# Performance work log

Hardware: AMD Instinct MI355X
Metric: run time of the kernel (lower is better)

Reference implementation:

```python
import jax, jax.numpy as jnp
import numpy as np

BN_EPS = 1e-5
LEAKY_SLOPE = 0.01

N_TOTAL, FEAT_DIM = 100000, 128
N_BATCH, K = 50000, 16
EMBED_DIM = 128


def setup_inputs() -> dict:
    key = jax.random.key(0)
    k1, k2, k3 = jax.random.split(key, 3)
    raw_features = jax.random.normal(k1, (N_TOTAL, FEAT_DIM), dtype=jnp.float32)
    weight = jax.random.normal(k2, (FEAT_DIM, EMBED_DIM), dtype=jnp.float32) * (1.0 / np.sqrt(FEAT_DIM))
    gamma = jnp.ones((EMBED_DIM,), dtype=jnp.float32)
    beta = jnp.zeros((EMBED_DIM,), dtype=jnp.float32)
    neigh_idx = jax.random.randint(k3, (N_BATCH, K), 0, N_TOTAL, dtype=jnp.int64)
    return {"raw_features": raw_features, "weight": weight, "gamma": gamma,
            "beta": beta, "neigh_idx": neigh_idx}


def reference(raw_features, weight, gamma, beta, neigh_idx):
    # Mean aggregation over sampled neighbors: [N_BATCH, K, F] -> [N_BATCH, F]
    neigh_feats = jnp.mean(raw_features[neigh_idx], axis=1)
    # Dense transform: [N_BATCH, EMBED_DIM]
    x = neigh_feats @ weight
    # BatchNorm1d (training mode: batch statistics, biased variance)
    mean = jnp.mean(x, axis=0)
    var = jnp.var(x, axis=0)
    x = (x - mean) * jax.lax.rsqrt(var + BN_EPS) * gamma + beta
    # LeakyReLU (default negative_slope=0.01)
    return jnp.where(x >= 0, x, LEAKY_SLOPE * x)
```

## Files before the change

### kernel.cpp

```cpp
#include <hip/hip_runtime.h>
#include <hip/hip_bf16.h>


#define NTOTAL 100000
#define FEAT   128
#define NB     50000
#define KNEI   16
#define NTILES (NB / 16)

#define OFF_STATS 0
#define OFF_WT    1024
#define OFF_RAWB  33792
#define OFF_XB    (33792 + 25600000)
#define WS_NEEDED (OFF_XB + 12800000)

typedef float f32x4 __attribute__((ext_vector_type(4)));
typedef short bf16x8 __attribute__((ext_vector_type(8)));

__device__ __forceinline__ unsigned short f2bf(float f) {
    union { float f; unsigned u; } v; v.f = f;
    unsigned r = v.u + 0x7FFF + ((v.u >> 16) & 1);
    return (unsigned short)(r >> 16);
}

#define WT_LD 136
#define A_LD  136

__global__ __launch_bounds__(256) void enc_conv(
    const float* __restrict__ raw, const float* __restrict__ W,
    unsigned short* __restrict__ rawb, unsigned short* __restrict__ Wt,
    float* __restrict__ gstats)
{
    const int t = threadIdx.x;
    if (blockIdx.x < 64) {
        int e = blockIdx.x * 256 + t;
        int n = e >> 7, k = e & 127;
        Wt[e] = f2bf(W[k * FEAT + n]);
    }
    if (blockIdx.x == 64 && t < 2 * FEAT) gstats[t] = 0.f;

    const float4* raw4 = (const float4*)raw;
    ushort4* rb4 = (ushort4*)rawb;
    const int NQ = NTOTAL * FEAT / 4;
    for (int e = blockIdx.x * 256 + t; e < NQ; e += gridDim.x * 256) {
        float4 v = raw4[e];
        ushort4 b;
        b.x = f2bf(v.x); b.y = f2bf(v.y); b.z = f2bf(v.z); b.w = f2bf(v.w);
        rb4[e] = b;
    }
}

__global__ __launch_bounds__(256, 4) void enc_gemm_b(
    const unsigned short* __restrict__ rawb, const unsigned short* __restrict__ Wt,
    const int* __restrict__ idx, unsigned short* __restrict__ xb,
    float* __restrict__ gstats)
{
    __shared__ unsigned short sWt[128 * WT_LD];
    __shared__ unsigned short sA[16 * A_LD];
    __shared__ int sidx[256];

    const int t = threadIdx.x;

    #pragma unroll
    for (int i = 0; i < 8; ++i) {
        int e = t + i * 256;
        int n = e >> 4, c = e & 15;
        *(uint4*)&sWt[n * WT_LD + c * 8] = *(const uint4*)&Wt[n * 128 + c * 8];
    }

    const int lane = t & 63;
    const int wv = t >> 6;
    const int ln = lane & 15;
    const int qd = lane >> 4;
    const int c2 = t & 15;
    const int g  = t >> 4;
    const int n0 = wv * 32 + ln, n1 = n0 + 16;

    float s1a = 0.f, s2a = 0.f, s1b = 0.f, s2b = 0.f;

    for (int tile = blockIdx.x; tile < NTILES; tile += gridDim.x) {
        const int i0 = tile * 16;
        __syncthreads();
        sidx[t] = idx[i0 * KNEI + t];
        __syncthreads();

        {
            const int* ip = &sidx[g * KNEI];
            uint4 v[16];
            #pragma unroll
            for (int k = 0; k < KNEI; ++k)
                v[k] = *(const uint4*)&rawb[(size_t)ip[k] * FEAT + c2 * 8];
            float a0=0.f,a1=0.f,a2=0.f,a3=0.f,a4=0.f,a5=0.f,a6=0.f,a7=0.f;
            #pragma unroll
            for (int k = 0; k < KNEI; ++k) {
                a0 += __uint_as_float(v[k].x << 16);
                a1 += __uint_as_float(v[k].x & 0xFFFF0000u);
                a2 += __uint_as_float(v[k].y << 16);
                a3 += __uint_as_float(v[k].y & 0xFFFF0000u);
                a4 += __uint_as_float(v[k].z << 16);
                a5 += __uint_as_float(v[k].z & 0xFFFF0000u);
                a6 += __uint_as_float(v[k].w << 16);
                a7 += __uint_as_float(v[k].w & 0xFFFF0000u);
            }
            uint4 b;
            b.x = (unsigned)f2bf(a0 * 0.0625f) | ((unsigned)f2bf(a1 * 0.0625f) << 16);
            b.y = (unsigned)f2bf(a2 * 0.0625f) | ((unsigned)f2bf(a3 * 0.0625f) << 16);
            b.z = (unsigned)f2bf(a4 * 0.0625f) | ((unsigned)f2bf(a5 * 0.0625f) << 16);
            b.w = (unsigned)f2bf(a6 * 0.0625f) | ((unsigned)f2bf(a7 * 0.0625f) << 16);
            *(uint4*)&sA[g * A_LD + c2 * 8] = b;
        }
        __syncthreads();

        f32x4 acc0 = {0.f, 0.f, 0.f, 0.f}, acc1 = {0.f, 0.f, 0.f, 0.f};
        #pragma unroll
        for (int kt = 0; kt < 4; ++kt) {
            const int k0 = kt * 32 + qd * 8;
            bf16x8 a  = *(const bf16x8*)&sA[ln * A_LD + k0];
            bf16x8 b0 = *(const bf16x8*)&sWt[n0 * WT_LD + k0];
            bf16x8 b1 = *(const bf16x8*)&sWt[n1 * WT_LD + k0];
            acc0 = __builtin_amdgcn_mfma_f32_16x16x32_bf16(a, b0, acc0, 0, 0, 0);
            acc1 = __builtin_amdgcn_mfma_f32_16x16x32_bf16(a, b1, acc1, 0, 0, 0);
        }

        #pragma unroll
        for (int ri = 0; ri < 4; ++ri) {
            const int row = i0 + qd * 4 + ri;
            float v0 = acc0[ri], v1 = acc1[ri];
            xb[row * FEAT + n0] = f2bf(v0);
            xb[row * FEAT + n1] = f2bf(v1);
            s1a += v0; s2a += v0 * v0;
            s1b += v1; s2b += v1 * v1;
        }
    }

    s1a += __shfl_down(s1a, 32); s1a += __shfl_down(s1a, 16);
    s2a += __shfl_down(s2a, 32); s2a += __shfl_down(s2a, 16);
    s1b += __shfl_down(s1b, 32); s1b += __shfl_down(s1b, 16);
    s2b += __shfl_down(s2b, 32); s2b += __shfl_down(s2b, 16);
    if (qd == 0) {
        atomicAdd(&gstats[n0], s1a);
        atomicAdd(&gstats[FEAT + n0], s2a);
        atomicAdd(&gstats[n1], s1b);
        atomicAdd(&gstats[FEAT + n1], s2b);
    }
}

__global__ __launch_bounds__(256) void enc_bn_b(
    const unsigned short* __restrict__ xb, float* __restrict__ out,
    const float* __restrict__ gstats,
    const float* __restrict__ gamma, const float* __restrict__ beta)
{
    __shared__ float sScale[FEAT], sShift[FEAT];
    const int t = threadIdx.x;
    if (t < FEAT) {
        float s1 = gstats[t], s2 = gstats[FEAT + t];
        float mean = s1 * (1.0f / NB);
        float var = s2 * (1.0f / NB) - mean * mean;
        float sc = gamma[t] * rsqrtf(var + 1e-5f);
        sScale[t] = sc;
        sShift[t] = beta[t] - mean * sc;
    }
    __syncthreads();

    const int f8 = (t & 15) * 8;
    const float4 sc0 = *(const float4*)&sScale[f8], sc1 = *(const float4*)&sScale[f8 + 4];
    const float4 sh0 = *(const float4*)&sShift[f8], sh1 = *(const float4*)&sShift[f8 + 4];

    const uint4* x4 = (const uint4*)xb;
    float4* o4 = (float4*)out;
    const int total8 = NB * FEAT / 8;
    for (int e = blockIdx.x * 256 + t; e < total8; e += gridDim.x * 256) {
        uint4 v = x4[e];
        float4 r0, r1; float y;
        y = __uint_as_float(v.x << 16)        * sc0.x + sh0.x; r0.x = (y >= 0.f) ? y : 0.01f * y;
        y = __uint_as_float(v.x & 0xFFFF0000u)* sc0.y + sh0.y; r0.y = (y >= 0.f) ? y : 0.01f * y;
        y = __uint_as_float(v.y << 16)        * sc0.z + sh0.z; r0.z = (y >= 0.f) ? y : 0.01f * y;
        y = __uint_as_float(v.y & 0xFFFF0000u)* sc0.w + sh0.w; r0.w = (y >= 0.f) ? y : 0.01f * y;
        y = __uint_as_float(v.z << 16)        * sc1.x + sh1.x; r1.x = (y >= 0.f) ? y : 0.01f * y;
        y = __uint_as_float(v.z & 0xFFFF0000u)* sc1.y + sh1.y; r1.y = (y >= 0.f) ? y : 0.01f * y;
        y = __uint_as_float(v.w << 16)        * sc1.z + sh1.z; r1.z = (y >= 0.f) ? y : 0.01f * y;
        y = __uint_as_float(v.w & 0xFFFF0000u)* sc1.w + sh1.w; r1.w = (y >= 0.f) ? y : 0.01f * y;
        o4[e * 2] = r0; o4[e * 2 + 1] = r1;
    }
}

__global__ __launch_bounds__(256, 4) void enc_gemm_f(
    const float* __restrict__ raw, const float* __restrict__ W,
    const int* __restrict__ idx, float* __restrict__ out,
    float* __restrict__ gstats)
{
    __shared__ unsigned short sWt[128 * WT_LD];
    __shared__ unsigned short sA[16 * A_LD];
    __shared__ int sidx[256];
    const int t = threadIdx.x;
    #pragma unroll 4
    for (int i = 0; i < 64; ++i) {
        int e = t + i * 256;
        int f = e >> 7, n = e & 127;
        sWt[n * WT_LD + f] = f2bf(W[e]);
    }
    const int lane = t & 63, wv = t >> 6, ln = lane & 15, qd = lane >> 4;
    const int c = t & 31, g = t >> 5;
    const int n0 = wv * 32 + ln, n1 = n0 + 16;
    float s1a = 0.f, s2a = 0.f, s1b = 0.f, s2b = 0.f;
    const float4* raw4 = (const float4*)raw;
    for (int tile = blockIdx.x; tile < NTILES; tile += gridDim.x) {
        const int i0 = tile * 16;
        __syncthreads();
        sidx[t] = idx[i0 * KNEI + t];
        __syncthreads();
        #pragma unroll
        for (int rr = 0; rr < 2; ++rr) {
            const int r = g * 2 + rr;
            const int* ip = &sidx[r * KNEI];
            float4 acc = {0.f, 0.f, 0.f, 0.f};
            #pragma unroll
            for (int k = 0; k < KNEI; ++k) {
                float4 v = raw4[(size_t)ip[k] * 32 + c];
                acc.x += v.x; acc.y += v.y; acc.z += v.z; acc.w += v.w;
            }
            ushort4 b;
            b.x = f2bf(acc.x * 0.0625f); b.y = f2bf(acc.y * 0.0625f);
            b.z = f2bf(acc.z * 0.0625f); b.w = f2bf(acc.w * 0.0625f);
            *(ushort4*)&sA[r * A_LD + c * 4] = b;
        }
        __syncthreads();
        f32x4 acc0 = {0.f, 0.f, 0.f, 0.f}, acc1 = {0.f, 0.f, 0.f, 0.f};
        #pragma unroll
        for (int kt = 0; kt < 4; ++kt) {
            const int k0 = kt * 32 + qd * 8;
            bf16x8 a  = *(const bf16x8*)&sA[ln * A_LD + k0];
            bf16x8 b0 = *(const bf16x8*)&sWt[n0 * WT_LD + k0];
            bf16x8 b1 = *(const bf16x8*)&sWt[n1 * WT_LD + k0];
            acc0 = __builtin_amdgcn_mfma_f32_16x16x32_bf16(a, b0, acc0, 0, 0, 0);
            acc1 = __builtin_amdgcn_mfma_f32_16x16x32_bf16(a, b1, acc1, 0, 0, 0);
        }
        #pragma unroll
        for (int ri = 0; ri < 4; ++ri) {
            const int row = i0 + qd * 4 + ri;
            float v0 = acc0[ri], v1 = acc1[ri];
            out[row * FEAT + n0] = v0;
            out[row * FEAT + n1] = v1;
            s1a += v0; s2a += v0 * v0;
            s1b += v1; s2b += v1 * v1;
        }
    }
    s1a += __shfl_down(s1a, 32); s1a += __shfl_down(s1a, 16);
    s2a += __shfl_down(s2a, 32); s2a += __shfl_down(s2a, 16);
    s1b += __shfl_down(s1b, 32); s1b += __shfl_down(s1b, 16);
    s2b += __shfl_down(s2b, 32); s2b += __shfl_down(s2b, 16);
    if (qd == 0) {
        atomicAdd(&gstats[n0], s1a);
        atomicAdd(&gstats[FEAT + n0], s2a);
        atomicAdd(&gstats[n1], s1b);
        atomicAdd(&gstats[FEAT + n1], s2b);
    }
}

__global__ __launch_bounds__(256) void enc_bn_f(
    float* __restrict__ out, const float* __restrict__ gstats,
    const float* __restrict__ gamma, const float* __restrict__ beta)
{
    __shared__ float sScale[FEAT], sShift[FEAT];
    const int t = threadIdx.x;
    if (t < FEAT) {
        float s1 = gstats[t], s2 = gstats[FEAT + t];
        float mean = s1 * (1.0f / NB);
        float var = s2 * (1.0f / NB) - mean * mean;
        float sc = gamma[t] * rsqrtf(var + 1e-5f);
        sScale[t] = sc;
        sShift[t] = beta[t] - mean * sc;
    }
    __syncthreads();
    const int f4 = (t & 31) * 4;
    const float4 sc = *(const float4*)&sScale[f4];
    const float4 sh = *(const float4*)&sShift[f4];
    const int total4 = NB * FEAT / 4;
    float4* o4 = (float4*)out;
    for (int e = blockIdx.x * 256 + t; e < total4; e += gridDim.x * 256) {
        float4 v = o4[e];
        float4 r; float y;
        y = v.x * sc.x + sh.x; r.x = (y >= 0.f) ? y : 0.01f * y;
        y = v.y * sc.y + sh.y; r.y = (y >= 0.f) ? y : 0.01f * y;
        y = v.z * sc.z + sh.z; r.z = (y >= 0.f) ? y : 0.01f * y;
        y = v.w * sc.w + sh.w; r.w = (y >= 0.f) ? y : 0.01f * y;
        o4[e] = r;
    }
}

extern "C" void kernel_launch(void* const* d_in, const int* in_sizes, int n_in,
                              void* d_out, int out_size, void* d_ws, size_t ws_size,
                              hipStream_t stream) {
    const float* raw   = (const float*)d_in[0];
    const float* W     = (const float*)d_in[1];
    const float* gamma = (const float*)d_in[2];
    const float* beta  = (const float*)d_in[3];
    const int*   idx   = (const int*)d_in[4];
    float* out = (float*)d_out;

    char* ws = (char*)d_ws;
    float* gstats = (float*)(ws + OFF_STATS);

    if (ws_size >= WS_NEEDED) {
        unsigned short* Wt   = (unsigned short*)(ws + OFF_WT);
        unsigned short* rawb = (unsigned short*)(ws + OFF_RAWB);
        unsigned short* xb   = (unsigned short*)(ws + OFF_XB);
        enc_conv<<<2048, 256, 0, stream>>>(raw, W, rawb, Wt, gstats);
        enc_gemm_b<<<1024, 256, 0, stream>>>(rawb, Wt, idx, xb, gstats);
        enc_bn_b<<<1024, 256, 0, stream>>>(xb, out, gstats, gamma, beta);
    } else {
        hipMemsetAsync(gstats, 0, 2 * FEAT * sizeof(float), stream);
        enc_gemm_f<<<1024, 256, 0, stream>>>(raw, W, idx, out, gstats);
        enc_bn_f<<<1024, 256, 0, stream>>>(out, gstats, gamma, beta);
    }
}
```

Baseline: 151.9 us.

## Split gather and GEMM into separate kernels using fp16 packed accumulation

Replaces the fused bf16 gather+GEMM kernel with a standalone gather kernel that sums neighbor rows with packed half2 adds (tree reduction) and writes fp16 neighbor means to workspace. A separate MFMA f16 GEMM kernel then holds the weights in registers, writes fp32 output directly, and accumulates BN statistics, and BN is applied in place. The goal is to cut ALU conversion work in the gather, avoid LDS syncs, and drop the bf16 intermediate of x. The cost is an extra kernel launch and an extra round trip of the neighbor-feature buffer. fp16 accumulation risks precision loss and overflow, and the in-place BN adds a read-modify-write of the fp32 output.

```diff
diff --git a/kernel.cpp b/kernel.cpp
--- a/kernel.cpp
+++ b/kernel.cpp
@@ -1,5 +1,6 @@
 #include <hip/hip_runtime.h>
 #include <hip/hip_bf16.h>
+#include <hip/hip_fp16.h>
 
 
 #define NTOTAL 100000
@@ -10,12 +11,13 @@
 
 #define OFF_STATS 0
 #define OFF_WT    1024
-#define OFF_RAWB  33792
-#define OFF_XB    (33792 + 25600000)
-#define WS_NEEDED (OFF_XB + 12800000)
+#define OFF_RAWH  33792
+#define OFF_NF    (33792 + 25600000)
+#define WS_NEEDED (OFF_NF + 12800000)
 
 typedef float f32x4 __attribute__((ext_vector_type(4)));
 typedef short bf16x8 __attribute__((ext_vector_type(8)));
+typedef _Float16 f16x8 __attribute__((ext_vector_type(8)));
 
 __device__ __forceinline__ unsigned short f2bf(float f) {
     union { float f; unsigned u; } v; v.f = f;
@@ -23,111 +25,117 @@
     return (unsigned short)(r >> 16);
 }
 
-#define WT_LD 136
-#define A_LD  136
+__device__ __forceinline__ unsigned h2add(unsigned a, unsigned b) {
+    union { unsigned u; __half2 h; } x, y, r;
+    x.u = a; y.u = b; r.h = __hadd2(x.h, y.h);
+    return r.u;
+}
+__device__ __forceinline__ unsigned h2scale16(unsigned a) {
+    union { unsigned u; __half2 h; } x, c, r;
+    x.u = a; c.u = 0x2C002C00u;
+    r.h = __hmul2(x.h, c.h);
+    return r.u;
+}
 
 __global__ __launch_bounds__(256) void enc_conv(
     const float* __restrict__ raw, const float* __restrict__ W,
-    unsigned short* __restrict__ rawb, unsigned short* __restrict__ Wt,
+    unsigned short* __restrict__ rawh, unsigned short* __restrict__ Wt,
     float* __restrict__ gstats)
 {
     const int t = threadIdx.x;
     if (blockIdx.x < 64) {
         int e = blockIdx.x * 256 + t;
         int n = e >> 7, k = e & 127;
-        Wt[e] = f2bf(W[k * FEAT + n]);
+        union { unsigned short s; __half h; } c; c.h = __float2half(W[k * FEAT + n]);
+        Wt[e] = c.s;
     }
     if (blockIdx.x == 64 && t < 2 * FEAT) gstats[t] = 0.f;
 
     const float4* raw4 = (const float4*)raw;
-    ushort4* rb4 = (ushort4*)rawb;
+    uint2* rh = (uint2*)rawh;
     const int NQ = NTOTAL * FEAT / 4;
     for (int e = blockIdx.x * 256 + t; e < NQ; e += gridDim.x * 256) {
         float4 v = raw4[e];
-        ushort4 b;
-        b.x = f2bf(v.x); b.y = f2bf(v.y); b.z = f2bf(v.z); b.w = f2bf(v.w);
-        rb4[e] = b;
-    }
-}
-
-__global__ __launch_bounds__(256, 4) void enc_gemm_b(
-    const unsigned short* __restrict__ rawb, const unsigned short* __restrict__ Wt,
-    const int* __restrict__ idx, unsigned short* __restrict__ xb,
-    float* __restrict__ gstats)
-{
-    __shared__ unsigned short sWt[128 * WT_LD];
-    __shared__ unsigned short sA[16 * A_LD];
-    __shared__ int sidx[256];
-
-    const int t = threadIdx.x;
-
+        union { unsigned u; __half2 h; } lo, hi;
+        lo.h = __float22half2_rn(make_float2(v.x, v.y));
+        hi.h = __float22half2_rn(make_float2(v.z, v.w));
+        uint2 o; o.x = lo.u; o.y = hi.u;
+        rh[e] = o;
+    }
+}
+
+__global__ __launch_bounds__(256, 5) void enc_gather(
+    const unsigned short* __restrict__ rawh, const int* __restrict__ idx,
+    unsigned short* __restrict__ nf)
+{
+    const int t = threadIdx.x;
+    const int lane = t & 63;
+    const int w = (blockIdx.x * 256 + t) >> 6;
+    const int r0 = w * 4;
+    const int s = lane >> 4, c = lane & 15;
+
+    const int iv = idx[r0 * KNEI + lane];
+
+    uint4 v[16];
     #pragma unroll
-    for (int i = 0; i < 8; ++i) {
-        int e = t + i * 256;
-        int n = e >> 4, c = e & 15;
-        *(uint4*)&sWt[n * WT_LD + c * 8] = *(const uint4*)&Wt[n * 128 + c * 8];
-    }
-
+    for (int k = 0; k < KNEI; ++k) {
+        int ik = __shfl(iv, s * 16 + k);
+        v[k] = *(const uint4*)&rawh[(size_t)ik * FEAT + c * 8];
+    }
+    #pragma unroll
+    for (int st = 8; st >= 1; st >>= 1) {
+        #pragma unroll
+        for (int k = 0; k < 8; ++k) {
+            if (k < st) {
+                v[k].x = h2add(v[k].x, v[k + st].x);
+                v[k].y = h2add(v[k].y, v[k + st].y);
+                v[k].z = h2add(v[k].z, v[k + st].z);
+                v[k].w = h2add(v[k].w, v[k + st].w);
+            }
+        }
+    }
+    uint4 o;
+    o.x = h2scale16(v[0].x); o.y = h2scale16(v[0].y);
+    o.z = h2scale16(v[0].z); o.w = h2scale16(v[0].w);
+    *(uint4*)&nf[(size_t)(r0 + s) * FEAT + c * 8] = o;
+}
+
+__global__ __launch_bounds__(256, 4) void enc_mm(
+    const unsigned short* __restrict__ nf, const unsigned short* __restrict__ Wt,
+    float* __restrict__ out, float* __restrict__ gstats)
+{
+    const int t = threadIdx.x;
     const int lane = t & 63;
     const int wv = t >> 6;
-    const int ln = lane & 15;
-    const int qd = lane >> 4;
-    const int c2 = t & 15;
-    const int g  = t >> 4;
+    const int ln = lane & 15, qd = lane >> 4;
     const int n0 = wv * 32 + ln, n1 = n0 + 16;
+
+    f16x8 b0[4], b1[4];
+    #pragma unroll
+    for (int kt = 0; kt < 4; ++kt) {
+        const int k0 = kt * 32 + qd * 8;
+        b0[kt] = *(const f16x8*)&Wt[n0 * FEAT + k0];
+        b1[kt] = *(const f16x8*)&Wt[n1 * FEAT + k0];
+    }
 
     float s1a = 0.f, s2a = 0.f, s1b = 0.f, s2b = 0.f;
 
     for (int tile = blockIdx.x; tile < NTILES; tile += gridDim.x) {
         const int i0 = tile * 16;
-        __syncthreads();
-        sidx[t] = idx[i0 * KNEI + t];
-        __syncthreads();
-
-        {
-            const int* ip = &sidx[g * KNEI];
-            uint4 v[16];
-            #pragma unroll
-            for (int k = 0; k < KNEI; ++k)
-                v[k] = *(const uint4*)&rawb[(size_t)ip[k] * FEAT + c2 * 8];
-            float a0=0.f,a1=0.f,a2=0.f,a3=0.f,a4=0.f,a5=0.f,a6=0.f,a7=0.f;
-            #pragma unroll
-            for (int k = 0; k < KNEI; ++k) {
-                a0 += __uint_as_float(v[k].x << 16);
-                a1 += __uint_as_float(v[k].x & 0xFFFF0000u);
-                a2 += __uint_as_float(v[k].y << 16);
-                a3 += __uint_as_float(v[k].y & 0xFFFF0000u);
-                a4 += __uint_as_float(v[k].z << 16);
-                a5 += __uint_as_float(v[k].z & 0xFFFF0000u);
-                a6 += __uint_as_float(v[k].w << 16);
-                a7 += __uint_as_float(v[k].w & 0xFFFF0000u);
-            }
-            uint4 b;
-            b.x = (unsigned)f2bf(a0 * 0.0625f) | ((unsigned)f2bf(a1 * 0.0625f) << 16);
-            b.y = (unsigned)f2bf(a2 * 0.0625f) | ((unsigned)f2bf(a3 * 0.0625f) << 16);
-            b.z = (unsigned)f2bf(a4 * 0.0625f) | ((unsigned)f2bf(a5 * 0.0625f) << 16);
-            b.w = (unsigned)f2bf(a6 * 0.0625f) | ((unsigned)f2bf(a7 * 0.0625f) << 16);
-            *(uint4*)&sA[g * A_LD + c2 * 8] = b;
-        }
-        __syncthreads();
-
         f32x4 acc0 = {0.f, 0.f, 0.f, 0.f}, acc1 = {0.f, 0.f, 0.f, 0.f};
         #pragma unroll
         for (int kt = 0; kt < 4; ++kt) {
             const int k0 = kt * 32 + qd * 8;
-            bf16x8 a  = *(const bf16x8*)&sA[ln * A_LD + k0];
-            bf16x8 b0 = *(const bf16x8*)&sWt[n0 * WT_LD + k0];
-            bf16x8 b1 = *(const bf16x8*)&sWt[n1 * WT_LD + k0];
-            acc0 = __builtin_amdgcn_mfma_f32_16x16x32_bf16(a, b0, acc0, 0, 0, 0);
-            acc1 = __builtin_amdgcn_mfma_f32_16x16x32_bf16(a, b1, acc1, 0, 0, 0);
-        }
-
+            f16x8 a = *(const f16x8*)&nf[(size_t)(i0 + ln) * FEAT + k0];
+            acc0 = __builtin_amdgcn_mfma_f32_16x16x32_f16(a, b0[kt], acc0, 0, 0, 0);
+            acc1 = __builtin_amdgcn_mfma_f32_16x16x32_f16(a, b1[kt], acc1, 0, 0, 0);
+        }
         #pragma unroll
         for (int ri = 0; ri < 4; ++ri) {
             const int row = i0 + qd * 4 + ri;
             float v0 = acc0[ri], v1 = acc1[ri];
-            xb[row * FEAT + n0] = f2bf(v0);
-            xb[row * FEAT + n1] = f2bf(v1);
+            out[row * FEAT + n0] = v0;
+            out[row * FEAT + n1] = v1;
             s1a += v0; s2a += v0 * v0;
             s1b += v1; s2b += v1 * v1;
         }
@@ -145,119 +153,7 @@
     }
 }
 
-__global__ __launch_bounds__(256) void enc_bn_b(
-    const unsigned short* __restrict__ xb, float* __restrict__ out,
-    const float* __restrict__ gstats,
-    const float* __restrict__ gamma, const float* __restrict__ beta)
-{
-    __shared__ float sScale[FEAT], sShift[FEAT];
-    const int t = threadIdx.x;
-    if (t < FEAT) {
-        float s1 = gstats[t], s2 = gstats[FEAT + t];
-        float mean = s1 * (1.0f / NB);
-        float var = s2 * (1.0f / NB) - mean * mean;
-        float sc = gamma[t] * rsqrtf(var + 1e-5f);
-        sScale[t] = sc;
-        sShift[t] = beta[t] - mean * sc;
-    }
-    __syncthreads();
-
-    const int f8 = (t & 15) * 8;
-    const float4 sc0 = *(const float4*)&sScale[f8], sc1 = *(const float4*)&sScale[f8 + 4];
-    const float4 sh0 = *(const float4*)&sShift[f8], sh1 = *(const float4*)&sShift[f8 + 4];
-
-    const uint4* x4 = (const uint4*)xb;
-    float4* o4 = (float4*)out;
-    const int total8 = NB * FEAT / 8;
-    for (int e = blockIdx.x * 256 + t; e < total8; e += gridDim.x * 256) {
-        uint4 v = x4[e];
-        float4 r0, r1; float y;
-        y = __uint_as_float(v.x << 16)        * sc0.x + sh0.x; r0.x = (y >= 0.f) ? y : 0.01f * y;
-        y = __uint_as_float(v.x & 0xFFFF0000u)* sc0.y + sh0.y; r0.y = (y >= 0.f) ? y : 0.01f * y;
-        y = __uint_as_float(v.y << 16)        * sc0.z + sh0.z; r0.z = (y >= 0.f) ? y : 0.01f * y;
-        y = __uint_as_float(v.y & 0xFFFF0000u)* sc0.w + sh0.w; r0.w = (y >= 0.f) ? y : 0.01f * y;
-        y = __uint_as_float(v.z << 16)        * sc1.x + sh1.x; r1.x = (y >= 0.f) ? y : 0.01f * y;
-        y = __uint_as_float(v.z & 0xFFFF0000u)* sc1.y + sh1.y; r1.y = (y >= 0.f) ? y : 0.01f * y;
-        y = __uint_as_float(v.w << 16)        * sc1.z + sh1.z; r1.z = (y >= 0.f) ? y : 0.01f * y;
-        y = __uint_as_float(v.w & 0xFFFF0000u)* sc1.w + sh1.w; r1.w = (y >= 0.f) ? y : 0.01f * y;
-        o4[e * 2] = r0; o4[e * 2 + 1] = r1;
-    }
-}
-
-__global__ __launch_bounds__(256, 4) void enc_gemm_f(
-    const float* __restrict__ raw, const float* __restrict__ W,
-    const int* __restrict__ idx, float* __restrict__ out,
-    float* __restrict__ gstats)
-{
-    __shared__ unsigned short sWt[128 * WT_LD];
-    __shared__ unsigned short sA[16 * A_LD];
-    __shared__ int sidx[256];
-    const int t = threadIdx.x;
-    #pragma unroll 4
-    for (int i = 0; i < 64; ++i) {
-        int e = t + i * 256;
-        int f = e >> 7, n = e & 127;
-        sWt[n * WT_LD + f] = f2bf(W[e]);
-    }
-    const int lane = t & 63, wv = t >> 6, ln = lane & 15, qd = lane >> 4;
-    const int c = t & 31, g = t >> 5;
-    const int n0 = wv * 32 + ln, n1 = n0 + 16;
-    float s1a = 0.f, s2a = 0.f, s1b = 0.f, s2b = 0.f;
-    const float4* raw4 = (const float4*)raw;
-    for (int tile = blockIdx.x; tile < NTILES; tile += gridDim.x) {
-        const int i0 = tile * 16;
-        __syncthreads();
-        sidx[t] = idx[i0 * KNEI + t];
-        __syncthreads();
-        #pragma unroll
-        for (int rr = 0; rr < 2; ++rr) {
-            const int r = g * 2 + rr;
-            const int* ip = &sidx[r * KNEI];
-            float4 acc = {0.f, 0.f, 0.f, 0.f};
-            #pragma unroll
-            for (int k = 0; k < KNEI; ++k) {
-                float4 v = raw4[(size_t)ip[k] * 32 + c];
-                acc.x += v.x; acc.y += v.y; acc.z += v.z; acc.w += v.w;
-            }
-            ushort4 b;
-            b.x = f2bf(acc.x * 0.0625f); b.y = f2bf(acc.y * 0.0625f);
-            b.z = f2bf(acc.z * 0.0625f); b.w = f2bf(acc.w * 0.0625f);
-            *(ushort4*)&sA[r * A_LD + c * 4] = b;
-        }
-        __syncthreads();
-        f32x4 acc0 = {0.f, 0.f, 0.f, 0.f}, acc1 = {0.f, 0.f, 0.f, 0.f};
-        #pragma unroll
-        for (int kt = 0; kt < 4; ++kt) {
-            const int k0 = kt * 32 + qd * 8;
-            bf16x8 a  = *(const bf16x8*)&sA[ln * A_LD + k0];
-            bf16x8 b0 = *(const bf16x8*)&sWt[n0 * WT_LD + k0];
-            bf16x8 b1 = *(const bf16x8*)&sWt[n1 * WT_LD + k0];
-            acc0 = __builtin_amdgcn_mfma_f32_16x16x32_bf16(a, b0, acc0, 0, 0, 0);
-            acc1 = __builtin_amdgcn_mfma_f32_16x16x32_bf16(a, b1, acc1, 0, 0, 0);
-        }
-        #pragma unroll
-        for (int ri = 0; ri < 4; ++ri) {
-            const int row = i0 + qd * 4 + ri;
-            float v0 = acc0[ri], v1 = acc1[ri];
-            out[row * FEAT + n0] = v0;
-            out[row * FEAT + n1] = v1;
-            s1a += v0; s2a += v0 * v0;
-            s1b += v1; s2b += v1 * v1;
-        }
-    }
-    s1a += __shfl_down(s1a, 32); s1a += __shfl_down(s1a, 16);
-    s2a += __shfl_down(s2a, 32); s2a += __shfl_down(s2a, 16);
-    s1b += __shfl_down(s1b, 32); s1b += __shfl_down(s1b, 16);
-    s2b += __shfl_down(s2b, 32); s2b += __shfl_down(s2b, 16);
-    if (qd == 0) {
-        atomicAdd(&gstats[n0], s1a);
-        atomicAdd(&gstats[FEAT + n0], s2a);
-        atomicAdd(&gstats[n1], s1b);
-        atomicAdd(&gstats[FEAT + n1], s2b);
-    }
-}
-
-__global__ __launch_bounds__(256) void enc_bn_f(
+__global__ __launch_bounds__(256) void enc_bn(
     float* __restrict__ out, const float* __restrict__ gstats,
     const float* __restrict__ gamma, const float* __restrict__ beta)
 {
@@ -288,6 +184,81 @@
     }
 }
 
+#define WT_LD 136
+#define A_LD  136
+__global__ __launch_bounds__(256, 4) void enc_gemm_f(
+    const float* __restrict__ raw, const float* __restrict__ W,
+    const int* __restrict__ idx, float* __restrict__ out,
+    float* __restrict__ gstats)
+{
+    __shared__ unsigned short sWt[128 * WT_LD];
+    __shared__ unsigned short sA[16 * A_LD];
+    __shared__ int sidx[256];
+    const int t = threadIdx.x;
+    #pragma unroll 4
+    for (int i = 0; i < 64; ++i) {
+        int e = t + i * 256;
+        int f = e >> 7, n = e & 127;
+        sWt[n * WT_LD + f] = f2bf(W[e]);
+    }
+    const int lane = t & 63, wv = t >> 6, ln = lane & 15, qd = lane >> 4;
+    const int c = t & 31, g = t >> 5;
+    const int n0 = wv * 32 + ln, n1 = n0 + 16;
+    float s1a = 0.f, s2a = 0.f, s1b = 0.f, s2b = 0.f;
+    const float4* raw4 = (const float4*)raw;
+    for (int tile = blockIdx.x; tile < NTILES; tile += gridDim.x) {
+        const int i0 = tile * 16;
+        __syncthreads();
+        sidx[t] = idx[i0 * KNEI + t];
+        __syncthreads();
+        #pragma unroll
+        for (int rr = 0; rr < 2; ++rr) {
+            const int r = g * 2 + rr;
+            const int* ip = &sidx[r * KNEI];
+            float4 acc = {0.f, 0.f, 0.f, 0.f};
+            #pragma unroll
+            for (int k = 0; k < KNEI; ++k) {
+                float4 v = raw4[(size_t)ip[k] * 32 + c];
+                acc.x += v.x; acc.y += v.y; acc.z += v.z; acc.w += v.w;
+            }
+            ushort4 b;
+            b.x = f2bf(acc.x * 0.0625f); b.y = f2bf(acc.y * 0.0625f);
+            b.z = f2bf(acc.z * 0.0625f); b.w = f2bf(acc.w * 0.0625f);
+            *(ushort4*)&sA[r * A_LD + c * 4] = b;
+        }
+        __syncthreads();
+        f32x4 acc0 = {0.f, 0.f, 0.f, 0.f}, acc1 = {0.f, 0.f, 0.f, 0.f};
+        #pragma unroll
+        for (int kt = 0; kt < 4; ++kt) {
+            const int k0 = kt * 32 + qd * 8;
+            bf16x8 a  = *(const bf16x8*)&sA[ln * A_LD + k0];
+            bf16x8 bb0 = *(const bf16x8*)&sWt[n0 * WT_LD + k0];
+            bf16x8 bb1 = *(const bf16x8*)&sWt[n1 * WT_LD + k0];
+            acc0 = __builtin_amdgcn_mfma_f32_16x16x32_bf16(a, bb0, acc0, 0, 0, 0);
+            acc1 = __builtin_amdgcn_mfma_f32_16x16x32_bf16(a, bb1, acc1, 0, 0, 0);
+        }
+        #pragma unroll
+        for (int ri = 0; ri < 4; ++ri) {
+            const int row = i0 + qd * 4 + ri;
+            float v0 = acc0[ri], v1 = acc1[ri];
+            out[row * FEAT + n0] = v0;
+            out[row * FEAT + n1] = v1;
+            s1a += v0; s2a += v0 * v0;
+            s1b += v1; s2b += v1 * v1;
+        }
+    }
+    s1a += __shfl_down(s1a, 32); s1a += __shfl_down(s1a, 16);
+    s2a += __shfl_down(s2a, 32); s2a += __shfl_down(s2a, 16);
+    s1b += __shfl_down(s1b, 32); s1b += __shfl_down(s1b, 16);
+    s2b += __shfl_down(s2b, 32); s2b += __shfl_down(s2b, 16);
+    if (qd == 0) {
+        atomicAdd(&gstats[n0], s1a);
+        atomicAdd(&gstats[FEAT + n0], s2a);
+        atomicAdd(&gstats[n1], s1b);
+        atomicAdd(&gstats[FEAT + n1], s2b);
+    }
+}
+
 extern "C" void kernel_launch(void* const* d_in, const int* in_sizes, int n_in,
                               void* d_out, int out_size, void* d_ws, size_t ws_size,
                               hipStream_t stream) {
@@ -303,14 +274,15 @@
 
     if (ws_size >= WS_NEEDED) {
         unsigned short* Wt   = (unsigned short*)(ws + OFF_WT);
-        unsigned short* rawb = (unsigned short*)(ws + OFF_RAWB);
-        unsigned short* xb   = (unsigned short*)(ws + OFF_XB);
-        enc_conv<<<2048, 256, 0, stream>>>(raw, W, rawb, Wt, gstats);
-        enc_gemm_b<<<1024, 256, 0, stream>>>(rawb, Wt, idx, xb, gstats);
-        enc_bn_b<<<1024, 256, 0, stream>>>(xb, out, gstats, gamma, beta);
+        unsigned short* rawh = (unsigned short*)(ws + OFF_RAWH);
+        unsigned short* nf   = (unsigned short*)(ws + OFF_NF);
+        enc_conv<<<2048, 256, 0, stream>>>(raw, W, rawh, Wt, gstats);
+        enc_gather<<<3125, 256, 0, stream>>>(rawh, idx, nf);
+        enc_mm<<<782, 256, 0, stream>>>(nf, Wt, out, gstats);
+        enc_bn<<<1024, 256, 0, stream>>>(out, gstats, gamma, beta);
     } else {
         hipMemsetAsync(gstats, 0, 2 * FEAT * sizeof(float), stream);
         enc_gemm_f<<<1024, 256, 0, stream>>>(raw, W, idx, out, gstats);
-        enc_bn_f<<<1024, 256, 0, stream>>>(out, gstats, gamma, beta);
-    }
-}
+        enc_bn<<<1024, 256, 0, stream>>>(out, gstats, gamma, beta);
+    }
+}
```

Result: slower. 163.9 us (+7.9%).
